# Performance work log

Measured on AMD Instinct MI355X. Metric: run time of the kernel, lower is better.

Reference implementation:

```python
import jax, jax.numpy as jnp
import numpy as np

DIM = 192
HEADS = 6
WIN = 8
SHIFT = 4
GROUPS = 8
MLP_HID = int(DIM * 4.0)
EPS = 1e-5


def setup_inputs() -> dict:
    key = jax.random.key(0)
    ks = jax.random.split(key, 14)
    s = lambda k, shape, fan: jax.random.normal(k, shape, jnp.float32) * (1.0 / np.sqrt(fan))
    return {
        "x": jax.random.normal(ks[0], (4, DIM, 256, 256), jnp.float32),
        # Linear weights stored [in, out] (transposed vs torch) for y = x @ W + b
        "qkv_w": s(ks[1], (DIM, 3 * DIM), DIM),
        "qkv_b": jnp.zeros((3 * DIM,), jnp.float32),
        "proj_w": s(ks[2], (DIM, DIM), DIM),
        "proj_b": jnp.zeros((DIM,), jnp.float32),
        "norm1_w": jnp.ones((DIM,), jnp.float32),
        "norm1_b": jnp.zeros((DIM,), jnp.float32),
        "norm2_w": jnp.ones((DIM,), jnp.float32),
        "norm2_b": jnp.zeros((DIM,), jnp.float32),
        "mlp_w1": s(ks[3], (DIM, MLP_HID), DIM),
        "mlp_b1": jnp.zeros((MLP_HID,), jnp.float32),
        "mlp_w2": s(ks[4], (MLP_HID, DIM), MLP_HID),
        "mlp_b2": jnp.zeros((DIM,), jnp.float32),
    }


def group_norm(x, w, b):  # x: [B,C,H,W]
    B, C, H, W = x.shape
    xg = x.reshape(B, GROUPS, (C // GROUPS) * H * W)
    mean = xg.mean(axis=-1, keepdims=True)
    var = xg.var(axis=-1, keepdims=True)
    xn = ((xg - mean) * jax.lax.rsqrt(var + EPS)).reshape(B, C, H, W)
    return xn * w[None, :, None, None] + b[None, :, None, None]


def window_partition(x):
    B, H, W, C = x.shape
    x = x.reshape(B, H // WIN, WIN, W // WIN, WIN, C)
    x = x.transpose(0, 1, 3, 2, 4, 5)
    return x.reshape(-1, WIN * WIN, C)


def window_reverse(win, H, W):
    C = win.shape[-1]
    B = win.shape[0] * WIN * WIN // (H * W)
    x = win.reshape(B, H // WIN, W // WIN, WIN, WIN, C)
    x = x.transpose(0, 1, 3, 2, 4, 5)
    return x.reshape(B, H, W, C)


def reference(x, qkv_w, qkv_b, proj_w, proj_b, norm1_w, norm1_b,
              norm2_w, norm2_b, mlp_w1, mlp_b1, mlp_w2, mlp_b2):
    B, C, H, W = x.shape
    hd = C // HEADS
    scale = hd ** -0.5

    # --- attention branch ---
    shortcut = x
    h = group_norm(x, norm1_w, norm1_b).transpose(0, 2, 3, 1)  # [B,H,W,C]
    h = jnp.roll(h, (-SHIFT, -SHIFT), axis=(1, 2))
    xw = window_partition(h)
    nW, N, _ = xw.shape
    qkv = (xw @ qkv_w + qkv_b).reshape(nW, N, 3, HEADS, hd)
    q, k, v = qkv[:, :, 0], qkv[:, :, 1], qkv[:, :, 2]  # [nW, N, h, d]
    attn = jnp.einsum('wnhd,wmhd->whnm', q * scale, k)
    attn = jax.nn.softmax(attn, axis=-1)
    o = jnp.einsum('whnm,wmhd->wnhd', attn, v).reshape(nW, N, C)
    o = o @ proj_w + proj_b
    h = window_reverse(o, H, W)
    h = jnp.roll(h, (SHIFT, SHIFT), axis=(1, 2))
    x = shortcut + h.transpose(0, 3, 1, 2)

    # --- MLP branch ---
    shortcut = x
    h = group_norm(x, norm2_w, norm2_b).transpose(0, 2, 3, 1).reshape(B, H * W, C)
    h = jax.nn.gelu(h @ mlp_w1 + mlp_b1, approximate=False) @ mlp_w2 + mlp_b2
    x = shortcut + h.reshape(B, H, W, C).transpose(0, 3, 1, 2)
    return x
```

## Files before the change

### kernel.cpp

```cpp
#include <hip/hip_runtime.h>

typedef unsigned short ushort_t;
typedef __bf16 bf16x8 __attribute__((ext_vector_type(8)));
typedef float f32x4 __attribute__((ext_vector_type(4)));
typedef unsigned short u16x8 __attribute__((ext_vector_type(8)));
typedef unsigned short u16x4 __attribute__((ext_vector_type(4)));

#define MFMA16(a, b, c) __builtin_amdgcn_mfma_f32_16x16x32_bf16(a, b, c, 0, 0, 0)

#define DIM 192
#define HEADS 6
#define GROUPS 8
#define CPG 24
#define HID 768
#define NWIN 4096
#define GN_N 1572864
#define SCALE 0.17677669529663687f

__device__ __forceinline__ ushort_t f2b(float f) {
  __bf16 h = (__bf16)f;
  return __builtin_bit_cast(unsigned short, h);
}
__device__ __forceinline__ float b2f(ushort_t u) {
  union { unsigned int u; float f; } v; v.u = ((unsigned int)u) << 16;
  return v.f;
}

__device__ __forceinline__ void xpose8(ushort_t V[8], int C3) {
#pragma unroll
  for (int bb = 0; bb < 3; ++bb) {
    const int m = 1 << bb;
    int tt[8];
#pragma unroll
    for (int j = 0; j < 8; ++j) tt[j] = __shfl_xor((int)V[j], m << 3, 64);
#pragma unroll
    for (int j = 0; j < 8; ++j)
      if (((j >> bb) & 1) != ((C3 >> bb) & 1)) V[j] = (ushort_t)tt[j ^ m];
  }
}

__global__ __launch_bounds__(256) void transpose_w(const float* __restrict__ in,
                                                   ushort_t* __restrict__ out,
                                                   int K, int N) {
  int id = blockIdx.x * 256 + threadIdx.x;
  if (id >= K * N) return;
  int n = id / K, k = id - n * K;
  out[id] = f2b(in[k * N + n]);
}

__global__ __launch_bounds__(256) void fold_w(
    const float* __restrict__ wsrc, const float* __restrict__ bsrc,
    const float* __restrict__ stats,
    const float* __restrict__ nw, const float* __restrict__ nb,
    ushort_t* __restrict__ wdst, float* __restrict__ bdst, int N) {
  int nb16 = N >> 4;
  int blk = blockIdx.x;
  int bb = blk / nb16, ng = blk - bb * nb16;
  int tid = threadIdx.x;
  int colL = tid >> 4, kq = tid & 15;
  int col = ng * 16 + colL;
  ushort_t* wout = wdst + ((size_t)bb * N + col) * 192;
  float acc = 0.f;
#pragma unroll
  for (int j = 0; j < 12; ++j) {
    int k = kq * 12 + j;
    int g = k / 24;
    float mean = stats[(bb * 8 + g) * 2], rstd = stats[(bb * 8 + g) * 2 + 1];
    float gw = nw[k] * rstd;
    float gb = nb[k] - mean * gw;
    float w_ = wsrc[(size_t)k * N + col];
    wout[k] = f2b(gw * w_);
    acc += gb * w_;
  }
  for (int m = 1; m < 16; m <<= 1) acc += __shfl_xor(acc, m);
  if (kq == 0) bdst[bb * N + col] = bsrc[col] + acc;
}

__global__ __launch_bounds__(64) void gn2_reduce(const float2* __restrict__ gpart,
                                                 float* __restrict__ stats) {
  int bid = blockIdx.x;
  int b = bid >> 3, g = bid & 7;
  int lane = threadIdx.x;
  float s = 0.f, s2 = 0.f;
  for (int w = lane; w < 1024; w += 64) {
    float2 v = gpart[((size_t)b * 1024 + w) * 8 + g];
    s += v.x; s2 += v.y;
  }
  for (int m = 1; m < 64; m <<= 1) { s += __shfl_xor(s, m); s2 += __shfl_xor(s2, m); }
  if (lane == 0) {
    const float invN = 1.0f / (float)GN_N;
    float mean = s * invN;
    float var = s2 * invN - mean * mean;
    stats[bid * 2] = mean;
    stats[bid * 2 + 1] = rsqrtf(var + 1e-5f);
  }
}

__global__ __launch_bounds__(256) void win_x(
    const float* __restrict__ x, ushort_t* __restrict__ buf,
    float2* __restrict__ gpart) {
  int w = blockIdx.x;
  int b = w >> 10, wh = (w >> 5) & 31, ww = w & 31;
  int tid = threadIdx.x;
  int wave = tid >> 6, lane = tid & 63;
  int C3 = lane >> 3, I = lane & 7;

  __shared__ __align__(16) ushort_t tile[64][200];

  int px0 = (ww << 3) + 4;
  int px1 = (px0 + 4) & 255;

#pragma unroll
  for (int it = 0; it < 6; ++it) {
    int u = it * 256 + tid;
    int c = u >> 3, i = u & 7;
    int py = ((wh << 3) + i + 4) & 255;
    const float* src = x + (((size_t)(b * DIM + c)) << 16) + (py << 8);
    float4 ra = *(const float4*)(src + px0);
    float4 rb = *(const float4*)(src + px1);
    ushort_t V[8];
    V[0] = f2b(ra.x); V[1] = f2b(ra.y); V[2] = f2b(ra.z); V[3] = f2b(ra.w);
    V[4] = f2b(rb.x); V[5] = f2b(rb.y); V[6] = f2b(rb.z); V[7] = f2b(rb.w);
    xpose8(V, C3);
    u16x8 wv;
#pragma unroll
    for (int j = 0; j < 8; ++j) wv[j] = V[j];
    int cbase = it * 32 + wave * 8;
    *(u16x8*)&tile[I * 8 + C3][cbase] = wv;
  }
  __syncthreads();

  ushort_t* bw = buf + (size_t)w * 12288;
  float sacc[6], s2acc[6];
#pragma unroll
  for (int it = 0; it < 6; ++it) {
    int u = it * 256 + tid;
    int token = u / 24, cv = u - token * 24;
    u16x8 v = *(const u16x8*)&tile[token][cv * 8];
    *(u16x8*)&bw[u * 8] = v;
    float s_ = 0.f, s2_ = 0.f;
#pragma unroll
    for (int t = 0; t < 8; ++t) { float f = b2f(v[t]); s_ += f; s2_ += f * f; }
    sacc[it] = s_; s2acc[it] = s2_;
  }
  __syncthreads();

  float2* red = (float2*)&tile[0][0];
#pragma unroll
  for (int it = 0; it < 6; ++it)
    red[it * 256 + tid] = make_float2(sacc[it], s2acc[it]);
  __syncthreads();

  for (int g = wave; g < 8; g += 4) {
    float s_ = 0.f, s2_ = 0.f;
#pragma unroll
    for (int j = 0; j < 3; ++j) {
      float2 t_ = red[lane * 24 + g * 3 + j];
      s_ += t_.x; s2_ += t_.y;
    }
    for (int m = 1; m < 64; m <<= 1) { s_ += __shfl_xor(s_, m); s2_ += __shfl_xor(s2_, m); }
    if (lane == 0) gpart[(size_t)w * 8 + g] = make_float2(s_, s2_);
  }
}

#define QKV_ATTN_PASS(PH)                                                      \
  {                                                                            \
    {                                                                          \
      int sec = wave >> 2;                                    \
      int tloc = wave & 3;                                                     \
      int cols16 = sec * 192 + (PH) * 64 + tloc * 16;                          \
      int lh = tloc >> 1;                                                      \
      int d = ((tloc & 1) << 4) + p;                                           \
      f32x4 acc0 = zz, acc1 = zz, acc2 = zz, acc3 = zz;                        \
      _Pragma("unroll")                                                        \
      for (int ks = 0; ks < 6; ++ks) {                                         \
        int k0 = ks * 32 + q8 * 8;                                             \
        bf16x8 bfr = *(const bf16x8*)(qkvT + (size_t)(cols16 + p) * DIM + k0); \
        acc0 = MFMA16(*(const bf16x8*)&tile[0 * 16 + p][k0], bfr, acc0);       \
        acc1 = MFMA16(*(const bf16x8*)&tile[1 * 16 + p][k0], bfr, acc1);       \
        acc2 = MFMA16(*(const bf16x8*)&tile[2 * 16 + p][k0], bfr, acc2);       \
        acc3 = MFMA16(*(const bf16x8*)&tile[3 * 16 + p][k0], bfr, acc3);       \
      }                                                                        \
      float bias = qkv_b[cols16 + p];                                          \
      if (sec == 0) {                                                          \
        int base = q8 * 4;                                                     \
        _Pragma("unroll")                                                      \
        for (int r = 0; r < 4; ++r) {                                          \
          qkP[lh][(0 * 16 + base + r) * 40 + d] = f2b((acc0[r] + bias) * SCALE); \
          qkP[lh][(1 * 16 + base + r) * 40 + d] = f2b((acc1[r] + bias) * SCALE); \
          qkP[lh][(2 * 16 + base + r) * 40 + d] = f2b((acc2[r] + bias) * SCALE); \
          qkP[lh][(3 * 16 + base + r) * 40 + d] = f2b((acc3[r] + bias) * SCALE); \
        }                                                                      \
      } else if (sec == 1) {                                                   \
        int base = q8 * 4;                                                     \
        _Pragma("unroll")                                                      \
        for (int r = 0; r < 4; ++r) {                                          \
          qkP[lh][2560 + (0 * 16 + base + r) * 40 + d] = f2b(acc0[r] + bias);  \
          qkP[lh][2560 + (1 * 16 + base + r) * 40 + d] = f2b(acc1[r] + bias);  \
          qkP[lh][2560 + (2 * 16 + base + r) * 40 + d] = f2b(acc2[r] + bias);  \
          qkP[lh][2560 + (3 * 16 + base + r) * 40 + d] = f2b(acc3[r] + bias);  \
        }                                                                      \
      } else {                                                                 \
        u16x4 v0, v1, v2, v3;                                                  \
        _Pragma("unroll")                                                      \
        for (int r = 0; r < 4; ++r) {                                          \
          v0[r] = f2b(acc0[r] + bias);                                         \
          v1[r] = f2b(acc1[r] + bias);                                         \
          v2[r] = f2b(acc2[r] + bias);                                         \
          v3[r] = f2b(acc3[r] + bias);                                         \
        }                                                                      \
        int base = d * 72 + q8 * 4;                                            \
        *(u16x4*)&vT[lh][base + 0]  = v0;                                      \
        *(u16x4*)&vT[lh][base + 16] = v1;                                      \
        *(u16x4*)&vT[lh][base + 32] = v2;                                      \
        *(u16x4*)&vT[lh][base + 48] = v3;                                      \
      }                                                                        \
    }                                                                          \
    __syncthreads();                                                   \
    {                                                                          \
      int lh = (wave >> 2) & 1, quad = wave & 3;                               \
      int rb_ = quad << 4;                                                     \
      int k0 = q8 * 8;                                                         \
      f32x4 s0 = zz, s1 = zz, s2 = zz, s3 = zz;                                \
      if (wave < 8) {                                                          \
        const ushort_t* qh = &qkP[lh][0];                                      \
        const ushort_t* kh = &qkP[lh][2560];                                   \
        bf16x8 aq = *(const bf16x8*)&qh[(rb_ + p) * 40 + k0];                  \
        bf16x8 bk0 = *(const bf16x8*)&kh[(0 + p) * 40 + k0];                   \
        bf16x8 bk1 = *(const bf16x8*)&kh[(16 + p) * 40 + k0];                  \
        bf16x8 bk2 = *(const bf16x8*)&kh[(32 + p) * 40 + k0];                  \
        bf16x8 bk3 = *(const bf16x8*)&kh[(48 + p) * 40 + k0];                  \
        s0 = MFMA16(aq, bk0, zz);                                              \
        s1 = MFMA16(aq, bk1, zz);                                              \
        s2 = MFMA16(aq, bk2, zz);                                              \
        s3 = MFMA16(aq, bk3, zz);                                              \
      }                                                                        \
      __syncthreads();              \
      if (wave < 8) {                                                          \
        ushort_t* Ph = &qkP[lh][0];                                            \
        _Pragma("unroll")                                                      \
        for (int r = 0; r < 4; ++r) {                                          \
          float m = fmaxf(fmaxf(s0[r], s1[r]), fmaxf(s2[r], s3[r]));           \
          for (int msk = 1; msk < 16; msk <<= 1) m = fmaxf(m, __shfl_xor(m, msk)); \
          float e0 = __expf(s0[r] - m);                                        \
          float e1 = __expf(s1[r] - m);                                        \
          float e2 = __expf(s2[r] - m);                                        \
          float e3 = __expf(s3[r] - m);                                        \
          float sum = e0 + e1 + e2 + e3;                                       \
          for (int msk = 1; msk < 16; msk <<= 1) sum += __shfl_xor(sum, msk);  \
          float inv = 1.0f / sum;                                              \
          int row = rb_ + q8 * 4 + r;                                          \
          Ph[row * 72 + 0 + p]  = f2b(e0 * inv);                               \
          Ph[row * 72 + 16 + p] = f2b(e1 * inv);                               \
          Ph[row * 72 + 32 + p] = f2b(e2 * inv);                               \
          Ph[row * 72 + 48 + p] = f2b(e3 * inv);                               \
        }                                                                      \
        f32x4 o0 = zz, o1 = zz;                                                \
        _Pragma("unroll")                                                      \
        for (int ks = 0; ks < 2; ++ks) {                                       \
          int kk = ks * 32 + k0;                                               \
          bf16x8 bv0 = *(const bf16x8*)&vT[lh][(0 + p) * 72 + kk];             \
          bf16x8 bv1 = *(const bf16x8*)&vT[lh][(16 + p) * 72 + kk];            \
          bf16x8 ap = *(const bf16x8*)&Ph[(rb_ + p) * 72 + kk];                \
          o0 = MFMA16(ap, bv0, o0);                                            \
          o1 = MFMA16(ap, bv1, o1);                                            \
        }                                                                      \
        size_t ob = (size_t)w * 12288 + (size_t)(rb_ + q8 * 4) * 192 +         \
                    ((PH) * 2 + lh) * 32 + p;                                  \
        _Pragma("unroll")                                                      \
        for (int r = 0; r < 4; ++r) {                                          \
          obuf[ob + (size_t)r * 192]      = f2b(o0[r]);                        \
          obuf[ob + (size_t)r * 192 + 16] = f2b(o1[r]);                        \
        }                                                                      \
      }                                                                        \
    }                                                                          \
  }

__global__ __launch_bounds__(768, 3) void attn_kernel(
    const ushort_t* __restrict__ buf_xn,
    const ushort_t* __restrict__ qkvTb_, const float* __restrict__ qkvbb_,
    ushort_t* __restrict__ obuf) {
  int w = blockIdx.x;
  int tid = threadIdx.x;
  int wave = tid >> 6, lane = tid & 63;
  int p = lane & 15, q8 = lane >> 4;

  const ushort_t* qkvT = qkvTb_ + (size_t)(w >> 10) * 110592;
  const float* qkv_b = qkvbb_ + (w >> 10) * 576;

  __shared__ __align__(16) ushort_t tile[64][200];
  __shared__ __align__(16) ushort_t qkP[2][5120];
  __shared__ __align__(16) ushort_t vT[2][2304];

  const ushort_t* bw = buf_xn + (size_t)w * 12288;
#pragma unroll
  for (int it = 0; it < 2; ++it) {
    int u = it * 768 + tid;
    int token = u / 24, cv = u - token * 24;
    *(u16x8*)&tile[token][cv * 8] = *(const u16x8*)&bw[u * 8];
  }
  __syncthreads();

  const f32x4 zz = {0.f, 0.f, 0.f, 0.f};

  QKV_ATTN_PASS(0)
  __syncthreads();
  QKV_ATTN_PASS(1)
  __syncthreads();
  QKV_ATTN_PASS(2)
}

__global__ __launch_bounds__(256) void proj_kernel(
    ushort_t* __restrict__ buf,
    const ushort_t* __restrict__ projT, const float* __restrict__ proj_b,
    const float* __restrict__ x, float2* __restrict__ gpart) {
  int w = blockIdx.x;
  int b = w >> 10, wh = (w >> 5) & 31, ww = w & 31;
  int tid = threadIdx.x;
  int wave = tid >> 6, lane = tid & 63;
  int p = lane & 15, q8 = lane >> 4;
  int C3 = lane >> 3, I = lane & 7;

  __shared__ __align__(16) ushort_t otile[64][200];

  ushort_t* bw = buf + (size_t)w * 12288;

#pragma unroll
  for (int it = 0; it < 6; ++it) {
    int idx = (it * 256 + tid) * 8;
    int t = idx / 192, c = idx - t * 192;
    *(u16x8*)&otile[t][c] = *(const u16x8*)&bw[idx];
  }
  __syncthreads();

  const f32x4 zz = {0.f, 0.f, 0.f, 0.f};
  f32x4 prr[3][4];
#pragma unroll
  for (int rd = 0; rd < 3; ++rd) {
    int col = rd * 64 + wave * 16 + p;
#pragma unroll
    for (int mt = 0; mt < 4; ++mt) prr[rd][mt] = zz;
#pragma unroll
    for (int ks = 0; ks < 6; ++ks) {
      int k0 = ks * 32 + q8 * 8;
      bf16x8 bfr = *(const bf16x8*)(projT + (size_t)col * DIM + k0);
      prr[rd][0] = MFMA16(*(const bf16x8*)&otile[0 * 16 + p][k0], bfr, prr[rd][0]);
      prr[rd][1] = MFMA16(*(const bf16x8*)&otile[1 * 16 + p][k0], bfr, prr[rd][1]);
      prr[rd][2] = MFMA16(*(const bf16x8*)&otile[2 * 16 + p][k0], bfr, prr[rd][2]);
      prr[rd][3] = MFMA16(*(const bf16x8*)&otile[3 * 16 + p][k0], bfr, prr[rd][3]);
    }
  }
  __syncthreads();

#pragma unroll
  for (int rd = 0; rd < 3; ++rd) {
    int col = rd * 64 + wave * 16 + p;
    float bias = proj_b[col];
#pragma unroll
    for (int mt = 0; mt < 4; ++mt)
#pragma unroll
      for (int r = 0; r < 4; ++r)
        otile[mt * 16 + q8 * 4 + r][col] = f2b(prr[rd][mt][r] + bias);
  }
  __syncthreads();

  int px0 = (ww << 3) + 4;
  int px1 = (px0 + 4) & 255;

#pragma unroll
  for (int it = 0; it < 6; ++it) {
    int u = it * 256 + tid;
    int c = u >> 3, i = u & 7;
    int cbase = it * 32 + wave * 8;
    u16x8 rr = *(const u16x8*)&otile[I * 8 + C3][cbase];
    ushort_t V[8];
#pragma unroll
    for (int j = 0; j < 8; ++j) V[j] = rr[j];
    xpose8(V, C3);
    int py = ((wh << 3) + i + 4) & 255;
    const float* src = x + (((size_t)(b * DIM + c)) << 16) + (py << 8);
    float4 ra = *(const float4*)(src + px0);
    V[0] = f2b(ra.x + b2f(V[0]));
    V[1] = f2b(ra.y + b2f(V[1]));
    V[2] = f2b(ra.z + b2f(V[2]));
    V[3] = f2b(ra.w + b2f(V[3]));
    float4 rb2 = *(const float4*)(src + px1);
    V[4] = f2b(rb2.x + b2f(V[4]));
    V[5] = f2b(rb2.y + b2f(V[5]));
    V[6] = f2b(rb2.z + b2f(V[6]));
    V[7] = f2b(rb2.w + b2f(V[7]));
    xpose8(V, C3);
    u16x8 wv;
#pragma unroll
    for (int j = 0; j < 8; ++j) wv[j] = V[j];
    *(u16x8*)&otile[I * 8 + C3][cbase] = wv;
  }
  __syncthreads();

  float sacc[6], s2acc[6];
#pragma unroll
  for (int it = 0; it < 6; ++it) {
    int u = it * 256 + tid;
    int token = u / 24, cv = u - token * 24;
    u16x8 v = *(const u16x8*)&otile[token][cv * 8];
    *(u16x8*)&bw[u * 8] = v;
    float s_ = 0.f, s2_ = 0.f;
#pragma unroll
    for (int t = 0; t < 8; ++t) { float f = b2f(v[t]); s_ += f; s2_ += f * f; }
    sacc[it] = s_; s2acc[it] = s2_;
  }
  __syncthreads();

  float2* red = (float2*)&otile[0][0];
#pragma unroll
  for (int it = 0; it < 6; ++it)
    red[it * 256 + tid] = make_float2(sacc[it], s2acc[it]);
  __syncthreads();

  for (int g = wave; g < 8; g += 4) {
    float s_ = 0.f, s2_ = 0.f;
#pragma unroll
    for (int j = 0; j < 3; ++j) {
      float2 t_ = red[lane * 24 + g * 3 + j];
      s_ += t_.x; s2_ += t_.y;
    }
    for (int m = 1; m < 64; m <<= 1) { s_ += __shfl_xor(s_, m); s2_ += __shfl_xor(s2_, m); }
    if (lane == 0) gpart[(size_t)w * 8 + g] = make_float2(s_, s2_);
  }
}

__global__ __launch_bounds__(256, 4) void mlp_kernel(
    const ushort_t* __restrict__ x_mid,
    const ushort_t* __restrict__ w1b, const float* __restrict__ b1b,
    const ushort_t* __restrict__ w2T, const float* __restrict__ b2,
    float* __restrict__ out) {
  int bid = blockIdx.x;
  int b = bid >> 10, y = (bid >> 2) & 255, xq = bid & 3;
  int x0 = xq * 64;
  int tid = threadIdx.x;
  int wave = tid >> 6, lane = tid & 63;
  int p = lane & 15, q = lane >> 4;

  __shared__ ushort_t xn[64][200];
  __shared__ ushort_t hb[64][72];

  const ushort_t* w1T = w1b + (size_t)b * 147456;
  const float* b1 = b1b + b * 768;

  int yp = (y + 252) & 255;
  int whp = yp >> 3, ip = yp & 7;
  size_t winrow = ((size_t)b * 1024 + (size_t)whp * 32) * 12288;

  for (int u = tid; u < 1536; u += 256) {
    int tx = u / 24, ch = u - tx * 24;
    int c8 = ch * 8;
    int xp = (x0 + tx + 252) & 255;
    *(u16x8*)&xn[tx][c8] =
        *(const u16x8*)(x_mid + winrow + (size_t)(xp >> 3) * 12288 +
                        (size_t)(ip * 8 + (xp & 7)) * 192 + c8);
  }
  __syncthreads();

  const f32x4 zz = {0.f, 0.f, 0.f, 0.f};
  f32x4 accO[4][3];
#pragma unroll
  for (int mt = 0; mt < 4; ++mt)
#pragma unroll
    for (int nt = 0; nt < 3; ++nt) accO[mt][nt] = zz;

  for (int ch = 0; ch < 12; ++ch) {
    int hcol16 = ch * 64 + wave * 16;
    f32x4 a1[4];
#pragma unroll
    for (int mt = 0; mt < 4; ++mt) a1[mt] = zz;
#pragma unroll
    for (int ks = 0; ks < 6; ++ks) {
      int k0 = ks * 32 + q * 8;
      bf16x8 wfr = *(const bf16x8*)(w1T + (size_t)(hcol16 + p) * DIM + k0);
#pragma unroll
      for (int mt = 0; mt < 4; ++mt) {
        bf16x8 afr = *(const bf16x8*)&xn[mt * 16 + p][k0];
        a1[mt] = MFMA16(wfr, afr, a1[mt]);
      }
    }
    float4 bb = *(const float4*)&b1[hcol16 + q * 4];
    if (ch) __syncthreads();
#pragma unroll
    for (int mt = 0; mt < 4; ++mt) {
      u16x4 hv;
#pragma unroll
      for (int r = 0; r < 4; ++r) {
        float vv = a1[mt][r] + ((const float*)&bb)[r];
        float g = vv / (1.0f + __expf(-1.702f * vv));
        hv[r] = f2b(g);
      }
      *(u16x4*)&hb[mt * 16 + p][wave * 16 + q * 4] = hv;
    }
    __syncthreads();
#pragma unroll
    for (int ks = 0; ks < 2; ++ks) {
      int k0 = ks * 32 + q * 8;
#pragma unroll
      for (int mt = 0; mt < 4; ++mt) {
        bf16x8 afr = *(const bf16x8*)&hb[mt * 16 + p][k0];
#pragma unroll
        for (int nt = 0; nt < 3; ++nt) {
          bf16x8 bfr = *(const bf16x8*)(w2T + (size_t)(wave * 48 + nt * 16 + p) * HID + ch * 64 + k0);
          accO[mt][nt] = MFMA16(afr, bfr, accO[mt][nt]);
        }
      }
    }
  }
  __syncthreads();

#pragma unroll
  for (int mt = 0; mt < 4; ++mt)
#pragma unroll
    for (int nt = 0; nt < 3; ++nt) {
      int col = wave * 48 + nt * 16 + p;
      float bias = b2[col];
#pragma unroll
      for (int r = 0; r < 4; ++r)
        xn[mt * 16 + q * 4 + r][col] = f2b(accO[mt][nt][r] + bias);
    }
  __syncthreads();

#pragma unroll
  for (int cg = 0; cg < 6; ++cg) {
    int chunk = (tid >> 6) + cg * 4;
    int txx = tid & 63;
    int c8 = chunk * 8;
    int xp = (x0 + txx + 252) & 255;
    u16x8 raw = *(const u16x8*)(x_mid + winrow + (size_t)(xp >> 3) * 12288 +
                                (size_t)(ip * 8 + (xp & 7)) * 192 + c8);
    u16x8 mo = *(const u16x8*)&xn[txx][c8];
#pragma unroll
    for (int t = 0; t < 8; ++t) {
      out[(((size_t)(b * DIM + c8 + t)) << 16) + (y << 8) + x0 + txx] =
          b2f(raw[t]) + b2f(mo[t]);
    }
  }
}

extern "C" void kernel_launch(void* const* d_in, const int* in_sizes, int n_in,
                              void* d_out, int out_size, void* d_ws, size_t ws_size,
                              hipStream_t stream) {
  const float* x      = (const float*)d_in[0];
  const float* qkv_w  = (const float*)d_in[1];
  const float* qkv_b  = (const float*)d_in[2];
  const float* proj_w = (const float*)d_in[3];
  const float* proj_b = (const float*)d_in[4];
  const float* n1w    = (const float*)d_in[5];
  const float* n1b    = (const float*)d_in[6];
  const float* n2w    = (const float*)d_in[7];
  const float* n2b    = (const float*)d_in[8];
  const float* mlp_w1 = (const float*)d_in[9];
  const float* mlp_b1 = (const float*)d_in[10];
  const float* mlp_w2 = (const float*)d_in[11];
  const float* mlp_b2 = (const float*)d_in[12];
  float* out = (float*)d_out;

  char* ws = (char*)d_ws;
  const size_t XMID_B = (size_t)NWIN * 64 * DIM * 2;
  ushort_t* buf   = (ushort_t*)ws;
  char* wp = ws + XMID_B;
  ushort_t* projT = (ushort_t*)(wp);
  ushort_t* w2T   = (ushort_t*)(wp + 73728);
  ushort_t* qkvTb = (ushort_t*)(wp + 368640);
  float*    qkvbb = (float*)   (wp + 1253376);
  ushort_t* w1b   = (ushort_t*)(wp + 1262592);
  float*    b1b   = (float*)   (wp + 2442240);
  float* stats1   = (float*)   (wp + 2454528);
  float* stats2   = (float*)   (wp + 2454784);
  float2* gpart   = (float2*)  (wp + 2455040);

  transpose_w<<<(192 * 192 + 255) / 256, 256, 0, stream>>>(proj_w, projT, 192, 192);
  transpose_w<<<(192 * 768 + 255) / 256, 256, 0, stream>>>(mlp_w2, w2T, 768, 192);

  win_x<<<NWIN, 256, 0, stream>>>(x, buf, gpart);

  gn2_reduce<<<32, 64, 0, stream>>>(gpart, stats1);

  fold_w<<<4 * 36, 256, 0, stream>>>(qkv_w, qkv_b, stats1, n1w, n1b,
                                     qkvTb, qkvbb, 576);

  attn_kernel<<<NWIN, 768, 0, stream>>>(buf, qkvTb, qkvbb, buf);

  proj_kernel<<<NWIN, 256, 0, stream>>>(buf, projT, proj_b, x, gpart);

  gn2_reduce<<<32, 64, 0, stream>>>(gpart, stats2);

  fold_w<<<4 * 48, 256, 0, stream>>>(mlp_w1, mlp_b1, stats2, n2w, n2b,
                                     w1b, b1b, 768);

  mlp_kernel<<<NWIN, 256, 0, stream>>>(buf, w1b, b1b, w2T, mlp_b2, out);
}
```

Measured before the change: 945.2 us.

## Use bf16 windowed residual in projection and reuse LDS tile for MLP residual

Adds a second projection kernel. The attention output goes to a separate workspace buffer, and the projection adds the residual from the already-windowed bf16 copy of x. Previously it gathered fp32 x from global memory with strided access. The MLP kernel now takes its residual from the shared-memory tile it already loaded instead of re-reading global memory. It also hoists the three w2 weight-fragment loads out of the inner tile loop. The new path needs extra workspace and falls back to the old kernels when the workspace is too small.

Result: faster. 767.4 us (-18.8%).

```diff
diff --git a/kernel.cpp b/kernel.cpp
--- a/kernel.cpp
+++ b/kernel.cpp
@@ -310,6 +310,97 @@
   QKV_ATTN_PASS(2)
 }
 
+__global__ __launch_bounds__(256) void proj_kernel2(
+    ushort_t* __restrict__ obuf, const ushort_t* __restrict__ xwin,
+    const ushort_t* __restrict__ projT, const float* __restrict__ proj_b,
+    float2* __restrict__ gpart) {
+  int w = blockIdx.x;
+  int tid = threadIdx.x;
+  int wave = tid >> 6, lane = tid & 63;
+  int p = lane & 15, q8 = lane >> 4;
+
+  __shared__ __align__(16) ushort_t otile[64][200];
+
+  ushort_t* bw = obuf + (size_t)w * 12288;
+  const ushort_t* xw = xwin + (size_t)w * 12288;
+
+#pragma unroll
+  for (int it = 0; it < 6; ++it) {
+    int idx = (it * 256 + tid) * 8;
+    int t = idx / 192, c = idx - t * 192;
+    *(u16x8*)&otile[t][c] = *(const u16x8*)&bw[idx];
+  }
+  __syncthreads();
+
+  const f32x4 zz = {0.f, 0.f, 0.f, 0.f};
+  f32x4 prr[3][4];
+#pragma unroll
+  for (int rd = 0; rd < 3; ++rd) {
+    int col = rd * 64 + wave * 16 + p;
+#pragma unroll
+    for (int mt = 0; mt < 4; ++mt) prr[rd][mt] = zz;
+#pragma unroll
+    for (int ks = 0; ks < 6; ++ks) {
+      int k0 = ks * 32 + q8 * 8;
+      bf16x8 bfr = *(const bf16x8*)(projT + (size_t)col * DIM + k0);
+      prr[rd][0] = MFMA16(*(const bf16x8*)&otile[0 * 16 + p][k0], bfr, prr[rd][0]);
+      prr[rd][1] = MFMA16(*(const bf16x8*)&otile[1 * 16 + p][k0], bfr, prr[rd][1]);
+      prr[rd][2] = MFMA16(*(const bf16x8*)&otile[2 * 16 + p][k0], bfr, prr[rd][2]);
+      prr[rd][3] = MFMA16(*(const bf16x8*)&otile[3 * 16 + p][k0], bfr, prr[rd][3]);
+    }
+  }
+  __syncthreads();
+
+#pragma unroll
+  for (int rd = 0; rd < 3; ++rd) {
+    int col = rd * 64 + wave * 16 + p;
+    float bias = proj_b[col];
+#pragma unroll
+    for (int mt = 0; mt < 4; ++mt)
+#pragma unroll
+      for (int r = 0; r < 4; ++r)
+        otile[mt * 16 + q8 * 4 + r][col] = f2b(prr[rd][mt][r] + bias);
+  }
+  __syncthreads();
+
+  float sacc[6], s2acc[6];
+#pragma unroll
+  for (int it = 0; it < 6; ++it) {
+    int u = it * 256 + tid;
+    int token = u / 24, cv = u - token * 24;
+    u16x8 ov = *(const u16x8*)&otile[token][cv * 8];
+    u16x8 xv = *(const u16x8*)&xw[u * 8];
+    u16x8 rv;
+    float s_ = 0.f, s2_ = 0.f;
+#pragma unroll
+    for (int t = 0; t < 8; ++t) {
+      rv[t] = f2b(b2f(ov[t]) + b2f(xv[t]));
+      float fb = b2f(rv[t]);
+      s_ += fb; s2_ += fb * fb;
+    }
+    *(u16x8*)&bw[u * 8] = rv;
+    sacc[it] = s_; s2acc[it] = s2_;
+  }
+  __syncthreads();
+
+  float2* red = (float2*)&otile[0][0];
+#pragma unroll
+  for (int it = 0; it < 6; ++it)
+    red[it * 256 + tid] = make_float2(sacc[it], s2acc[it]);
+  __syncthreads();
+
+  for (int g = wave; g < 8; g += 4) {
+    float s_ = 0.f, s2_ = 0.f;
+#pragma unroll
+    for (int j = 0; j < 3; ++j) {
+      float2 t_ = red[lane * 24 + g * 3 + j];
+      s_ += t_.x; s2_ += t_.y;
+    }
+    for (int m = 1; m < 64; m <<= 1) { s_ += __shfl_xor(s_, m); s2_ += __shfl_xor(s2_, m); }
+    if (lane == 0) gpart[(size_t)w * 8 + g] = make_float2(s_, s2_);
+  }
+}
+
 __global__ __launch_bounds__(256) void proj_kernel(
     ushort_t* __restrict__ buf,
     const ushort_t* __restrict__ projT, const float* __restrict__ proj_b,
@@ -500,16 +591,23 @@
 #pragma unroll
     for (int ks = 0; ks < 2; ++ks) {
       int k0 = ks * 32 + q * 8;
+      bf16x8 w20 = *(const bf16x8*)(w2T + (size_t)(wave * 48 + 0 * 16 + p) * HID + ch * 64 + k0);
+      bf16x8 w21 = *(const bf16x8*)(w2T + (size_t)(wave * 48 + 1 * 16 + p) * HID + ch * 64 + k0);
+      bf16x8 w22 = *(const bf16x8*)(w2T + (size_t)(wave * 48 + 2 * 16 + p) * HID + ch * 64 + k0);
 #pragma unroll
       for (int mt = 0; mt < 4; ++mt) {
         bf16x8 afr = *(const bf16x8*)&hb[mt * 16 + p][k0];
-#pragma unroll
-        for (int nt = 0; nt < 3; ++nt) {
-          bf16x8 bfr = *(const bf16x8*)(w2T + (size_t)(wave * 48 + nt * 16 + p) * HID + ch * 64 + k0);
-          accO[mt][nt] = MFMA16(afr, bfr, accO[mt][nt]);
-        }
+        accO[mt][0] = MFMA16(afr, w20, accO[mt][0]);
+        accO[mt][1] = MFMA16(afr, w21, accO[mt][1]);
+        accO[mt][2] = MFMA16(afr, w22, accO[mt][2]);
       }
     }
+  }
+  u16x8 raws[6];
+#pragma unroll
+  for (int cg = 0; cg < 6; ++cg) {
+    int chunk = (tid >> 6) + cg * 4;
+    raws[cg] = *(const u16x8*)&xn[tid & 63][chunk * 8];
   }
   __syncthreads();
 
@@ -530,9 +628,7 @@
     int chunk = (tid >> 6) + cg * 4;
     int txx = tid & 63;
     int c8 = chunk * 8;
-    int xp = (x0 + txx + 252) & 255;
-    u16x8 raw = *(const u16x8*)(x_mid + winrow + (size_t)(xp >> 3) * 12288 +
-                                (size_t)(ip * 8 + (xp & 7)) * 192 + c8);
+    u16x8 raw = raws[cg];
     u16x8 mo = *(const u16x8*)&xn[txx][c8];
 #pragma unroll
     for (int t = 0; t < 8; ++t) {
@@ -562,6 +658,7 @@
 
   char* ws = (char*)d_ws;
   const size_t XMID_B = (size_t)NWIN * 64 * DIM * 2;
+  const size_t WP_B   = 2717184;
   ushort_t* buf   = (ushort_t*)ws;
   char* wp = ws + XMID_B;
   ushort_t* projT = (ushort_t*)(wp);
@@ -573,6 +670,8 @@
   float* stats1   = (float*)   (wp + 2454528);
   float* stats2   = (float*)   (wp + 2454784);
   float2* gpart   = (float2*)  (wp + 2455040);
+  ushort_t* buf2  = (ushort_t*)(wp + WP_B);
+  bool two = ws_size >= XMID_B + WP_B + XMID_B;
 
   transpose_w<<<(192 * 192 + 255) / 256, 256, 0, stream>>>(proj_w, projT, 192, 192);
   transpose_w<<<(192 * 768 + 255) / 256, 256, 0, stream>>>(mlp_w2, w2T, 768, 192);
@@ -584,14 +683,18 @@
   fold_w<<<4 * 36, 256, 0, stream>>>(qkv_w, qkv_b, stats1, n1w, n1b,
                                      qkvTb, qkvbb, 576);
 
-  attn_kernel<<<NWIN, 768, 0, stream>>>(buf, qkvTb, qkvbb, buf);
-
-  proj_kernel<<<NWIN, 256, 0, stream>>>(buf, projT, proj_b, x, gpart);
+  if (two) {
+    attn_kernel<<<NWIN, 768, 0, stream>>>(buf, qkvTb, qkvbb, buf2);
+    proj_kernel2<<<NWIN, 256, 0, stream>>>(buf2, buf, projT, proj_b, gpart);
+  } else {
+    attn_kernel<<<NWIN, 768, 0, stream>>>(buf, qkvTb, qkvbb, buf);
+    proj_kernel<<<NWIN, 256, 0, stream>>>(buf, projT, proj_b, x, gpart);
+  }
 
   gn2_reduce<<<32, 64, 0, stream>>>(gpart, stats2);
 
   fold_w<<<4 * 48, 256, 0, stream>>>(mlp_w1, mlp_b1, stats2, n2w, n2b,
                                      w1b, b1b, 768);
 
-  mlp_kernel<<<NWIN, 256, 0, stream>>>(buf, w1b, b1b, w2T, mlp_b2, out);
-}
+  mlp_kernel<<<NWIN, 256, 0, stream>>>(two ? buf2 : buf, w1b, b1b, w2T, mlp_b2, out);
+}
```

## Read windowed bf16 residual in proj and widen MLP kernel to twelve waves

Applied to the files above, without the earlier changes.

The projection kernel now writes its output to a separate buffer. It takes the residual from the already windowed bf16 copy of x, instead of gathering fp32 x from NCHW with in-register 8x8 transposes, which cuts strided global reads and shuffle work. The MLP kernel moves to 768 threads, processes the hidden dimension in 4 chunks of 192 with 16 output columns per wave, and reuses the residual held in LDS instead of reloading it from global memory. In exchange the residual add loses fp32 precision for x, workspace grows by one buffer, and the (768, 8) launch bound may squeeze registers and risk spills.

Measured after the change: 856.3 us. 9.4% less time.

```diff
diff --git a/kernel.cpp b/kernel.cpp
--- a/kernel.cpp
+++ b/kernel.cpp
@@ -310,20 +310,19 @@
   QKV_ATTN_PASS(2)
 }
 
-__global__ __launch_bounds__(256) void proj_kernel(
-    ushort_t* __restrict__ buf,
+__global__ __launch_bounds__(256) void proj_kernel2(
+    ushort_t* __restrict__ obuf, const ushort_t* __restrict__ xwin,
     const ushort_t* __restrict__ projT, const float* __restrict__ proj_b,
-    const float* __restrict__ x, float2* __restrict__ gpart) {
+    float2* __restrict__ gpart) {
   int w = blockIdx.x;
-  int b = w >> 10, wh = (w >> 5) & 31, ww = w & 31;
   int tid = threadIdx.x;
   int wave = tid >> 6, lane = tid & 63;
   int p = lane & 15, q8 = lane >> 4;
-  int C3 = lane >> 3, I = lane & 7;
 
   __shared__ __align__(16) ushort_t otile[64][200];
 
-  ushort_t* bw = buf + (size_t)w * 12288;
+  ushort_t* bw = obuf + (size_t)w * 12288;
+  const ushort_t* xw = xwin + (size_t)w * 12288;
 
 #pragma unroll
   for (int it = 0; it < 6; ++it) {
@@ -364,49 +363,22 @@
   }
   __syncthreads();
 
-  int px0 = (ww << 3) + 4;
-  int px1 = (px0 + 4) & 255;
-
-#pragma unroll
-  for (int it = 0; it < 6; ++it) {
-    int u = it * 256 + tid;
-    int c = u >> 3, i = u & 7;
-    int cbase = it * 32 + wave * 8;
-    u16x8 rr = *(const u16x8*)&otile[I * 8 + C3][cbase];
-    ushort_t V[8];
-#pragma unroll
-    for (int j = 0; j < 8; ++j) V[j] = rr[j];
-    xpose8(V, C3);
-    int py = ((wh << 3) + i + 4) & 255;
-    const float* src = x + (((size_t)(b * DIM + c)) << 16) + (py << 8);
-    float4 ra = *(const float4*)(src + px0);
-    V[0] = f2b(ra.x + b2f(V[0]));
-    V[1] = f2b(ra.y + b2f(V[1]));
-    V[2] = f2b(ra.z + b2f(V[2]));
-    V[3] = f2b(ra.w + b2f(V[3]));
-    float4 rb2 = *(const float4*)(src + px1);
-    V[4] = f2b(rb2.x + b2f(V[4]));
-    V[5] = f2b(rb2.y + b2f(V[5]));
-    V[6] = f2b(rb2.z + b2f(V[6]));
-    V[7] = f2b(rb2.w + b2f(V[7]));
-    xpose8(V, C3);
-    u16x8 wv;
-#pragma unroll
-    for (int j = 0; j < 8; ++j) wv[j] = V[j];
-    *(u16x8*)&otile[I * 8 + C3][cbase] = wv;
-  }
-  __syncthreads();
-
   float sacc[6], s2acc[6];
 #pragma unroll
   for (int it = 0; it < 6; ++it) {
     int u = it * 256 + tid;
     int token = u / 24, cv = u - token * 24;
-    u16x8 v = *(const u16x8*)&otile[token][cv * 8];
-    *(u16x8*)&bw[u * 8] = v;
+    u16x8 ov = *(const u16x8*)&otile[token][cv * 8];
+    u16x8 xv = *(const u16x8*)&xw[u * 8];
+    u16x8 rv;
     float s_ = 0.f, s2_ = 0.f;
 #pragma unroll
-    for (int t = 0; t < 8; ++t) { float f = b2f(v[t]); s_ += f; s2_ += f * f; }
+    for (int t = 0; t < 8; ++t) {
+      rv[t] = f2b(b2f(ov[t]) + b2f(xv[t]));
+      float fb = b2f(rv[t]);
+      s_ += fb; s2_ += fb * fb;
+    }
+    *(u16x8*)&bw[u * 8] = rv;
     sacc[it] = s_; s2acc[it] = s2_;
   }
   __syncthreads();
@@ -429,7 +401,7 @@
   }
 }
 
-__global__ __launch_bounds__(256, 4) void mlp_kernel(
+__global__ __launch_bounds__(768, 8) void mlp_kernel(
     const ushort_t* __restrict__ x_mid,
     const ushort_t* __restrict__ w1b, const float* __restrict__ b1b,
     const ushort_t* __restrict__ w2T, const float* __restrict__ b2,
@@ -442,7 +414,7 @@
   int p = lane & 15, q = lane >> 4;
 
   __shared__ ushort_t xn[64][200];
-  __shared__ ushort_t hb[64][72];
+  __shared__ ushort_t hb[64][200];
 
   const ushort_t* w1T = w1b + (size_t)b * 147456;
   const float* b1 = b1b + b * 768;
@@ -451,7 +423,9 @@
   int whp = yp >> 3, ip = yp & 7;
   size_t winrow = ((size_t)b * 1024 + (size_t)whp * 32) * 12288;
 
-  for (int u = tid; u < 1536; u += 256) {
+#pragma unroll
+  for (int it = 0; it < 2; ++it) {
+    int u = it * 768 + tid;
     int tx = u / 24, ch = u - tx * 24;
     int c8 = ch * 8;
     int xp = (x0 + tx + 252) & 255;
@@ -462,81 +436,94 @@
   __syncthreads();
 
   const f32x4 zz = {0.f, 0.f, 0.f, 0.f};
-  f32x4 accO[4][3];
-#pragma unroll
-  for (int mt = 0; mt < 4; ++mt)
-#pragma unroll
-    for (int nt = 0; nt < 3; ++nt) accO[mt][nt] = zz;
-
-  for (int ch = 0; ch < 12; ++ch) {
-    int hcol16 = ch * 64 + wave * 16;
-    f32x4 a1[4];
-#pragma unroll
-    for (int mt = 0; mt < 4; ++mt) a1[mt] = zz;
+  f32x4 accO0 = zz, accO1 = zz, accO2 = zz, accO3 = zz;
+
+#pragma unroll
+  for (int ch = 0; ch < 4; ++ch) {
+    int hbase = ch * 192 + wave * 16;
+    f32x4 a10 = zz, a11 = zz, a12 = zz, a13 = zz;
 #pragma unroll
     for (int ks = 0; ks < 6; ++ks) {
       int k0 = ks * 32 + q * 8;
-      bf16x8 wfr = *(const bf16x8*)(w1T + (size_t)(hcol16 + p) * DIM + k0);
-#pragma unroll
-      for (int mt = 0; mt < 4; ++mt) {
-        bf16x8 afr = *(const bf16x8*)&xn[mt * 16 + p][k0];
-        a1[mt] = MFMA16(wfr, afr, a1[mt]);
+      bf16x8 wfr = *(const bf16x8*)(w1T + (size_t)(hbase + p) * DIM + k0);
+      a10 = MFMA16(wfr, *(const bf16x8*)&xn[0 * 16 + p][k0], a10);
+      a11 = MFMA16(wfr, *(const bf16x8*)&xn[1 * 16 + p][k0], a11);
+      a12 = MFMA16(wfr, *(const bf16x8*)&xn[2 * 16 + p][k0], a12);
+      a13 = MFMA16(wfr, *(const bf16x8*)&xn[3 * 16 + p][k0], a13);
+    }
+    float4 bb = *(const float4*)&b1[hbase + q * 4];
+    if (ch) __syncthreads();
+    {
+      int hc = wave * 16 + q * 4;
+      u16x4 hv;
+#pragma unroll
+      for (int r = 0; r < 4; ++r) {
+        float vv = a10[r] + ((const float*)&bb)[r];
+        hv[r] = f2b(vv / (1.0f + __expf(-1.702f * vv)));
       }
-    }
-    float4 bb = *(const float4*)&b1[hcol16 + q * 4];
-    if (ch) __syncthreads();
-#pragma unroll
-    for (int mt = 0; mt < 4; ++mt) {
-      u16x4 hv;
+      *(u16x4*)&hb[0 * 16 + p][hc] = hv;
 #pragma unroll
       for (int r = 0; r < 4; ++r) {
-        float vv = a1[mt][r] + ((const float*)&bb)[r];
-        float g = vv / (1.0f + __expf(-1.702f * vv));
-        hv[r] = f2b(g);
+        float vv = a11[r] + ((const float*)&bb)[r];
+        hv[r] = f2b(vv / (1.0f + __expf(-1.702f * vv)));
       }
-      *(u16x4*)&hb[mt * 16 + p][wave * 16 + q * 4] = hv;
+      *(u16x4*)&hb[1 * 16 + p][hc] = hv;
+#pragma unroll
+      for (int r = 0; r < 4; ++r) {
+        float vv = a12[r] + ((const float*)&bb)[r];
+        hv[r] = f2b(vv / (1.0f + __expf(-1.702f * vv)));
+      }
+      *(u16x4*)&hb[2 * 16 + p][hc] = hv;
+#pragma unroll
+      for (int r = 0; r < 4; ++r) {
+        float vv = a13[r] + ((const float*)&bb)[r];
+        hv[r] = f2b(vv / (1.0f + __expf(-1.702f * vv)));
+      }
+      *(u16x4*)&hb[3 * 16 + p][hc] = hv;
     }
     __syncthreads();
 #pragma unroll
-    for (int ks = 0; ks < 2; ++ks) {
+    for (int ks = 0; ks < 6; ++ks) {
       int k0 = ks * 32 + q * 8;
-#pragma unroll
-      for (int mt = 0; mt < 4; ++mt) {
-        bf16x8 afr = *(const bf16x8*)&hb[mt * 16 + p][k0];
-#pragma unroll
-        for (int nt = 0; nt < 3; ++nt) {
-          bf16x8 bfr = *(const bf16x8*)(w2T + (size_t)(wave * 48 + nt * 16 + p) * HID + ch * 64 + k0);
-          accO[mt][nt] = MFMA16(afr, bfr, accO[mt][nt]);
-        }
-      }
-    }
-  }
-  __syncthreads();
-
-#pragma unroll
-  for (int mt = 0; mt < 4; ++mt)
-#pragma unroll
-    for (int nt = 0; nt < 3; ++nt) {
-      int col = wave * 48 + nt * 16 + p;
-      float bias = b2[col];
-#pragma unroll
-      for (int r = 0; r < 4; ++r)
-        xn[mt * 16 + q * 4 + r][col] = f2b(accO[mt][nt][r] + bias);
-    }
-  __syncthreads();
-
-#pragma unroll
-  for (int cg = 0; cg < 6; ++cg) {
-    int chunk = (tid >> 6) + cg * 4;
-    int txx = tid & 63;
+      bf16x8 w2f = *(const bf16x8*)(w2T + (size_t)(wave * 16 + p) * HID + ch * 192 + k0);
+      accO0 = MFMA16(w2f, *(const bf16x8*)&hb[0 * 16 + p][k0], accO0);
+      accO1 = MFMA16(w2f, *(const bf16x8*)&hb[1 * 16 + p][k0], accO1);
+      accO2 = MFMA16(w2f, *(const bf16x8*)&hb[2 * 16 + p][k0], accO2);
+      accO3 = MFMA16(w2f, *(const bf16x8*)&hb[3 * 16 + p][k0], accO3);
+    }
+  }
+  u16x8 raw0 = *(const u16x8*)&xn[lane][(wave * 2 + 0) * 8];
+  u16x8 raw1 = *(const u16x8*)&xn[lane][(wave * 2 + 1) * 8];
+  __syncthreads();
+
+  {
+    float4 bb2 = *(const float4*)&b2[wave * 16 + q * 4];
+    int oc = wave * 16 + q * 4;
+    u16x4 ov;
+#pragma unroll
+    for (int r = 0; r < 4; ++r) ov[r] = f2b(accO0[r] + ((const float*)&bb2)[r]);
+    *(u16x4*)&xn[0 * 16 + p][oc] = ov;
+#pragma unroll
+    for (int r = 0; r < 4; ++r) ov[r] = f2b(accO1[r] + ((const float*)&bb2)[r]);
+    *(u16x4*)&xn[1 * 16 + p][oc] = ov;
+#pragma unroll
+    for (int r = 0; r < 4; ++r) ov[r] = f2b(accO2[r] + ((const float*)&bb2)[r]);
+    *(u16x4*)&xn[2 * 16 + p][oc] = ov;
+#pragma unroll
+    for (int r = 0; r < 4; ++r) ov[r] = f2b(accO3[r] + ((const float*)&bb2)[r]);
+    *(u16x4*)&xn[3 * 16 + p][oc] = ov;
+  }
+  __syncthreads();
+
+#pragma unroll
+  for (int cg = 0; cg < 2; ++cg) {
+    int chunk = wave * 2 + cg;
     int c8 = chunk * 8;
-    int xp = (x0 + txx + 252) & 255;
-    u16x8 raw = *(const u16x8*)(x_mid + winrow + (size_t)(xp >> 3) * 12288 +
-                                (size_t)(ip * 8 + (xp & 7)) * 192 + c8);
-    u16x8 mo = *(const u16x8*)&xn[txx][c8];
+    u16x8 raw = cg ? raw1 : raw0;
+    u16x8 mo = *(const u16x8*)&xn[lane][c8];
 #pragma unroll
     for (int t = 0; t < 8; ++t) {
-      out[(((size_t)(b * DIM + c8 + t)) << 16) + (y << 8) + x0 + txx] =
+      out[(((size_t)(b * DIM + c8 + t)) << 16) + (y << 8) + x0 + lane] =
           b2f(raw[t]) + b2f(mo[t]);
     }
   }
@@ -562,6 +549,7 @@
 
   char* ws = (char*)d_ws;
   const size_t XMID_B = (size_t)NWIN * 64 * DIM * 2;
+  const size_t WP_B   = 2717184;
   ushort_t* buf   = (ushort_t*)ws;
   char* wp = ws + XMID_B;
   ushort_t* projT = (ushort_t*)(wp);
@@ -573,6 +561,7 @@
   float* stats1   = (float*)   (wp + 2454528);
   float* stats2   = (float*)   (wp + 2454784);
   float2* gpart   = (float2*)  (wp + 2455040);
+  ushort_t* buf2  = (ushort_t*)(wp + WP_B);
 
   transpose_w<<<(192 * 192 + 255) / 256, 256, 0, stream>>>(proj_w, projT, 192, 192);
   transpose_w<<<(192 * 768 + 255) / 256, 256, 0, stream>>>(mlp_w2, w2T, 768, 192);
@@ -584,14 +573,14 @@
   fold_w<<<4 * 36, 256, 0, stream>>>(qkv_w, qkv_b, stats1, n1w, n1b,
                                      qkvTb, qkvbb, 576);
 
-  attn_kernel<<<NWIN, 768, 0, stream>>>(buf, qkvTb, qkvbb, buf);
-
-  proj_kernel<<<NWIN, 256, 0, stream>>>(buf, projT, proj_b, x, gpart);
+  attn_kernel<<<NWIN, 768, 0, stream>>>(buf, qkvTb, qkvbb, buf2);
+
+  proj_kernel2<<<NWIN, 256, 0, stream>>>(buf2, buf, projT, proj_b, gpart);
 
   gn2_reduce<<<32, 64, 0, stream>>>(gpart, stats2);
 
   fold_w<<<4 * 48, 256, 0, stream>>>(mlp_w1, mlp_b1, stats2, n2w, n2b,
                                      w1b, b1b, 768);
 
-  mlp_kernel<<<NWIN, 256, 0, stream>>>(buf, w1b, b1b, w2T, mlp_b2, out);
-}
+  mlp_kernel<<<NWIN, 768, 0, stream>>>(buf2, w1b, b1b, w2T, mlp_b2, out);
+}
```

## Take attention residual from windowed bf16 buffer and reuse MLP residual from shared memory

Applied to the files above, without the earlier changes.

Attention output now goes to a second workspace buffer. The projection kernel adds the residual by reading the already windowed bf16 copy of x contiguously, instead of gathering the shifted fp32 input with strided loads and 8x8 register transposes. In the MLP kernel the residual is taken from the x_mid tile already in shared memory rather than re-gathered from global memory, and the w2 fragments are hoisted out of the inner M-tile loop. This cuts global traffic and shuffle work, but the residual now uses bf16-rounded x instead of fp32 x, and an extra workspace buffer is needed.

Result: faster. 769.0 us (median of 2 runs) (-18.6%).

```diff
diff --git a/kernel.cpp b/kernel.cpp
--- a/kernel.cpp
+++ b/kernel.cpp
@@ -310,20 +310,19 @@
   QKV_ATTN_PASS(2)
 }
 
-__global__ __launch_bounds__(256) void proj_kernel(
-    ushort_t* __restrict__ buf,
+__global__ __launch_bounds__(256) void proj_kernel2(
+    ushort_t* __restrict__ obuf, const ushort_t* __restrict__ xwin,
     const ushort_t* __restrict__ projT, const float* __restrict__ proj_b,
-    const float* __restrict__ x, float2* __restrict__ gpart) {
+    float2* __restrict__ gpart) {
   int w = blockIdx.x;
-  int b = w >> 10, wh = (w >> 5) & 31, ww = w & 31;
   int tid = threadIdx.x;
   int wave = tid >> 6, lane = tid & 63;
   int p = lane & 15, q8 = lane >> 4;
-  int C3 = lane >> 3, I = lane & 7;
 
   __shared__ __align__(16) ushort_t otile[64][200];
 
-  ushort_t* bw = buf + (size_t)w * 12288;
+  ushort_t* bw = obuf + (size_t)w * 12288;
+  const ushort_t* xw = xwin + (size_t)w * 12288;
 
 #pragma unroll
   for (int it = 0; it < 6; ++it) {
@@ -364,49 +363,22 @@
   }
   __syncthreads();
 
-  int px0 = (ww << 3) + 4;
-  int px1 = (px0 + 4) & 255;
-
-#pragma unroll
-  for (int it = 0; it < 6; ++it) {
-    int u = it * 256 + tid;
-    int c = u >> 3, i = u & 7;
-    int cbase = it * 32 + wave * 8;
-    u16x8 rr = *(const u16x8*)&otile[I * 8 + C3][cbase];
-    ushort_t V[8];
-#pragma unroll
-    for (int j = 0; j < 8; ++j) V[j] = rr[j];
-    xpose8(V, C3);
-    int py = ((wh << 3) + i + 4) & 255;
-    const float* src = x + (((size_t)(b * DIM + c)) << 16) + (py << 8);
-    float4 ra = *(const float4*)(src + px0);
-    V[0] = f2b(ra.x + b2f(V[0]));
-    V[1] = f2b(ra.y + b2f(V[1]));
-    V[2] = f2b(ra.z + b2f(V[2]));
-    V[3] = f2b(ra.w + b2f(V[3]));
-    float4 rb2 = *(const float4*)(src + px1);
-    V[4] = f2b(rb2.x + b2f(V[4]));
-    V[5] = f2b(rb2.y + b2f(V[5]));
-    V[6] = f2b(rb2.z + b2f(V[6]));
-    V[7] = f2b(rb2.w + b2f(V[7]));
-    xpose8(V, C3);
-    u16x8 wv;
-#pragma unroll
-    for (int j = 0; j < 8; ++j) wv[j] = V[j];
-    *(u16x8*)&otile[I * 8 + C3][cbase] = wv;
-  }
-  __syncthreads();
-
   float sacc[6], s2acc[6];
 #pragma unroll
   for (int it = 0; it < 6; ++it) {
     int u = it * 256 + tid;
     int token = u / 24, cv = u - token * 24;
-    u16x8 v = *(const u16x8*)&otile[token][cv * 8];
-    *(u16x8*)&bw[u * 8] = v;
+    u16x8 ov = *(const u16x8*)&otile[token][cv * 8];
+    u16x8 xv = *(const u16x8*)&xw[u * 8];
+    u16x8 rv;
     float s_ = 0.f, s2_ = 0.f;
 #pragma unroll
-    for (int t = 0; t < 8; ++t) { float f = b2f(v[t]); s_ += f; s2_ += f * f; }
+    for (int t = 0; t < 8; ++t) {
+      rv[t] = f2b(b2f(ov[t]) + b2f(xv[t]));
+      float fb = b2f(rv[t]);
+      s_ += fb; s2_ += fb * fb;
+    }
+    *(u16x8*)&bw[u * 8] = rv;
     sacc[it] = s_; s2acc[it] = s2_;
   }
   __syncthreads();
@@ -500,16 +472,23 @@
 #pragma unroll
     for (int ks = 0; ks < 2; ++ks) {
       int k0 = ks * 32 + q * 8;
+      bf16x8 w20 = *(const bf16x8*)(w2T + (size_t)(wave * 48 + 0 * 16 + p) * HID + ch * 64 + k0);
+      bf16x8 w21 = *(const bf16x8*)(w2T + (size_t)(wave * 48 + 1 * 16 + p) * HID + ch * 64 + k0);
+      bf16x8 w22 = *(const bf16x8*)(w2T + (size_t)(wave * 48 + 2 * 16 + p) * HID + ch * 64 + k0);
 #pragma unroll
       for (int mt = 0; mt < 4; ++mt) {
         bf16x8 afr = *(const bf16x8*)&hb[mt * 16 + p][k0];
-#pragma unroll
-        for (int nt = 0; nt < 3; ++nt) {
-          bf16x8 bfr = *(const bf16x8*)(w2T + (size_t)(wave * 48 + nt * 16 + p) * HID + ch * 64 + k0);
-          accO[mt][nt] = MFMA16(afr, bfr, accO[mt][nt]);
-        }
+        accO[mt][0] = MFMA16(afr, w20, accO[mt][0]);
+        accO[mt][1] = MFMA16(afr, w21, accO[mt][1]);
+        accO[mt][2] = MFMA16(afr, w22, accO[mt][2]);
       }
     }
+  }
+  u16x8 raws[6];
+#pragma unroll
+  for (int cg = 0; cg < 6; ++cg) {
+    int chunk = (tid >> 6) + cg * 4;
+    raws[cg] = *(const u16x8*)&xn[tid & 63][chunk * 8];
   }
   __syncthreads();
 
@@ -530,9 +509,7 @@
     int chunk = (tid >> 6) + cg * 4;
     int txx = tid & 63;
     int c8 = chunk * 8;
-    int xp = (x0 + txx + 252) & 255;
-    u16x8 raw = *(const u16x8*)(x_mid + winrow + (size_t)(xp >> 3) * 12288 +
-                                (size_t)(ip * 8 + (xp & 7)) * 192 + c8);
+    u16x8 raw = raws[cg];
     u16x8 mo = *(const u16x8*)&xn[txx][c8];
 #pragma unroll
     for (int t = 0; t < 8; ++t) {
@@ -562,6 +539,7 @@
 
   char* ws = (char*)d_ws;
   const size_t XMID_B = (size_t)NWIN * 64 * DIM * 2;
+  const size_t WP_B   = 2717184;
   ushort_t* buf   = (ushort_t*)ws;
   char* wp = ws + XMID_B;
   ushort_t* projT = (ushort_t*)(wp);
@@ -573,6 +551,7 @@
   float* stats1   = (float*)   (wp + 2454528);
   float* stats2   = (float*)   (wp + 2454784);
   float2* gpart   = (float2*)  (wp + 2455040);
+  ushort_t* buf2  = (ushort_t*)(wp + WP_B);
 
   transpose_w<<<(192 * 192 + 255) / 256, 256, 0, stream>>>(proj_w, projT, 192, 192);
   transpose_w<<<(192 * 768 + 255) / 256, 256, 0, stream>>>(mlp_w2, w2T, 768, 192);
@@ -584,14 +563,14 @@
   fold_w<<<4 * 36, 256, 0, stream>>>(qkv_w, qkv_b, stats1, n1w, n1b,
                                      qkvTb, qkvbb, 576);
 
-  attn_kernel<<<NWIN, 768, 0, stream>>>(buf, qkvTb, qkvbb, buf);
-
-  proj_kernel<<<NWIN, 256, 0, stream>>>(buf, projT, proj_b, x, gpart);
+  attn_kernel<<<NWIN, 768, 0, stream>>>(buf, qkvTb, qkvbb, buf2);
+
+  proj_kernel2<<<NWIN, 256, 0, stream>>>(buf2, buf, projT, proj_b, gpart);
 
   gn2_reduce<<<32, 64, 0, stream>>>(gpart, stats2);
 
   fold_w<<<4 * 48, 256, 0, stream>>>(mlp_w1, mlp_b1, stats2, n2w, n2b,
                                      w1b, b1b, 768);
 
-  mlp_kernel<<<NWIN, 256, 0, stream>>>(buf, w1b, b1b, w2T, mlp_b2, out);
-}
+  mlp_kernel<<<NWIN, 256, 0, stream>>>(buf2, w1b, b1b, w2T, mlp_b2, out);
+}
```
